# Kernel optimization log

Hardware: AMD Instinct MI355X
Metric: run time of the kernel (lower is better)

The kernel has to match this reference:

```python
import jax, jax.numpy as jnp
import numpy as np

P, B, D, H, O = 512, 8, 256, 75, 128  # passage_len, batch, input_size, attn hidden, GRU hidden


def setup_inputs() -> dict:
    key = jax.random.key(0)
    ks = jax.random.split(key, 10)

    def w(k, shape, fan_in):
        return jax.random.normal(k, shape, jnp.float32) * (1.0 / np.sqrt(fan_in))

    return {
        "v": jax.random.normal(ks[0], (P, B, D), jnp.float32),
        "Wvp1": w(ks[1], (H, D), D),          # nn.Linear(input_size, hidden, bias=False)
        "Wvp2": w(ks[2], (H, D), D),
        "vw": w(ks[3], (H,), H),               # nn.Linear(hidden, 1, bias=False)
        "Wg": w(ks[4], (2 * D, 2 * D), 2 * D),  # Gate linear, no bias
        "w_ih_f": w(ks[5], (3 * O, 2 * D), 2 * D),
        "w_hh_f": w(ks[6], (3 * O, O), O),
        "b_ih_f": jnp.zeros((3 * O,), jnp.float32),
        "b_hh_f": jnp.zeros((3 * O,), jnp.float32),
        "w_ih_b": w(ks[7], (3 * O, 2 * D), 2 * D),
        "w_hh_b": w(ks[8], (3 * O, O), O),
        "b_ih_b": jnp.zeros((3 * O,), jnp.float32),
        "b_hh_b": jnp.zeros((3 * O,), jnp.float32),
    }


def _gru(x, w_ih, w_hh, b_ih, b_hh):
    # x: (T, B, in) -> hidden states (T, B, O); PyTorch GRU gate order (r, z, n)
    hdim = w_hh.shape[1]
    xp = x @ w_ih.T + b_ih  # precompute input projections: (T, B, 3O)

    def step(h, xp_t):
        gh = h @ w_hh.T + b_hh
        i_r, i_z, i_n = jnp.split(xp_t, 3, axis=-1)
        h_r, h_z, h_n = jnp.split(gh, 3, axis=-1)
        r = jax.nn.sigmoid(i_r + h_r)
        z = jax.nn.sigmoid(i_z + h_z)
        n = jnp.tanh(i_n + r * h_n)
        h_new = (1.0 - z) * n + z * h
        return h_new, h_new

    h0 = jnp.zeros((x.shape[1], hdim), x.dtype)
    _, hs = jax.lax.scan(step, h0, xp)
    return hs


def reference(v, Wvp1, Wvp2, vw, Wg,
              w_ih_f, w_hh_f, b_ih_f, b_hh_f,
              w_ih_b, w_hh_b, b_ih_b, b_hh_b):
    # dropout is inference no-op (and in the torch code its result is discarded anyway)
    Wv1 = v @ Wvp1.T  # (P, B, H) -- broadcast over key axis (dim 1 after expand)
    Wv2 = v @ Wvp2.T  # (P, B, H) -- broadcast over query axis
    # s[i, j, b, h] = tanh(Wv2[i] + Wv1[j]); softmax over i (keys)
    s = jnp.tanh(Wv2[:, None] + Wv1[None, :])          # (P, P, B, H)
    scores = jnp.einsum('ijbh,h->ijb', s, vw)          # (P, P, B)
    a = jax.nn.softmax(scores, axis=0)
    c = jnp.einsum('ijb,ibd->jbd', a, v)               # attended context (P, B, D)
    g = jnp.concatenate([v, c], axis=2)                # (P, B, 2D)
    g = jax.nn.sigmoid(g @ Wg.T) * g                   # Gate
    hf = _gru(g, w_ih_f, w_hh_f, b_ih_f, b_hh_f)
    hb = _gru(g[::-1], w_ih_b, w_hh_b, b_ih_b, b_hh_b)[::-1]
    return jnp.concatenate([hf, hb], axis=2)           # (P, B, 2O)
```

## Files before the change

kernel.cpp:

```cpp
#include <hip/hip_runtime.h>

#define TP 512
#define TB 8
#define TD 256
#define TH 75
#define THP 80
#define TO 128

typedef _Float16 half_t;
typedef _Float16 half2v __attribute__((ext_vector_type(2)));
typedef _Float16 half4v __attribute__((ext_vector_type(4)));
typedef _Float16 half8v __attribute__((ext_vector_type(8)));
typedef float    float4v __attribute__((ext_vector_type(4)));

__device__ __forceinline__ float fast_rcp(float x) { return __builtin_amdgcn_rcpf(x); }
__device__ __forceinline__ float fast_tanh(float x) {
    return 1.0f - 2.0f * fast_rcp(1.0f + __expf(2.0f * x));
}
__device__ __forceinline__ float fast_sigmoid(float x) {
    return fast_rcp(1.0f + __expf(-x));
}
__device__ __forceinline__ float fdot2h(half2v a, half2v b, float c) {
#if __has_builtin(__builtin_amdgcn_fdot2)
    return __builtin_amdgcn_fdot2(a, b, c, false);
#else
    return c + (float)a[0] * (float)b[0] + (float)a[1] * (float)b[1];
#endif
}
#define EXT2(v, j) __builtin_shufflevector((v), (v), 2*(j), 2*(j)+1)
__device__ __forceinline__ void dot3_h8(half8v wr, half8v wz, half8v wn, half8v h,
                                        float& ar, float& az, float& an) {
    half2v h0 = EXT2(h, 0), h1 = EXT2(h, 1), h2 = EXT2(h, 2), h3 = EXT2(h, 3);
    ar = fdot2h(EXT2(wr, 0), h0, ar);
    az = fdot2h(EXT2(wz, 0), h0, az);
    an = fdot2h(EXT2(wn, 0), h0, an);
    ar = fdot2h(EXT2(wr, 1), h1, ar);
    az = fdot2h(EXT2(wz, 1), h1, az);
    an = fdot2h(EXT2(wn, 1), h1, an);
    ar = fdot2h(EXT2(wr, 2), h2, ar);
    az = fdot2h(EXT2(wz, 2), h2, az);
    an = fdot2h(EXT2(wn, 2), h2, an);
    ar = fdot2h(EXT2(wr, 3), h3, ar);
    az = fdot2h(EXT2(wz, 3), h3, az);
    an = fdot2h(EXT2(wn, 3), h3, an);
}
__device__ __forceinline__ float pair_sum_dpp(float v) {
    int i1 = __builtin_amdgcn_update_dpp(0, __builtin_bit_cast(int, v), 0xB1, 0xF, 0xF, true);
    return v + __builtin_bit_cast(float, i1);
}

__global__ __launch_bounds__(256) void prep_kernel(
    const float* __restrict__ v,
    const float* __restrict__ Wvp1, const float* __restrict__ Wvp2,
    const float* __restrict__ Wg,   const float* __restrict__ wihf,
    const float* __restrict__ wihb, const float* __restrict__ bihf,
    const float* __restrict__ bihb, const float* __restrict__ whhf,
    const float* __restrict__ whhb,
    float* __restrict__ bihC,
    half_t* __restrict__ v16, half_t* __restrict__ g16,
    half_t* __restrict__ Wg16B, half_t* __restrict__ Wih16B,
    half_t* __restrict__ whh16, half_t* __restrict__ WT16B)
{
    int idx = blockIdx.x * 256 + threadIdx.x;
    if (idx < 1048576) {
        half_t val = (half_t)v[idx];
        v16[idx] = val;
        int row = idx >> 8, d = idx & 255;
        g16[row * 512 + d] = val;
        return;
    }
    idx -= 1048576;
    if (idx < 768) { bihC[idx] = (idx < 384) ? bihf[idx] : bihb[idx - 384]; return; }
    idx -= 768;
    if (idx < 262144) {
        int j = idx & 7, lane = (idx >> 3) & 63, kt = (idx >> 9) & 15, nt = idx >> 13;
        int o = nt * 16 + (lane & 15);
        int k = kt * 32 + ((lane >> 4) << 3) + j;
        Wg16B[idx] = (half_t)Wg[o * 512 + k];
        return;
    }
    idx -= 262144;
    if (idx < 393216) {
        int j = idx & 7, lane = (idx >> 3) & 63, kt = (idx >> 9) & 15, nt = idx >> 13;
        int o = nt * 16 + (lane & 15);
        int k = kt * 32 + ((lane >> 4) << 3) + j;
        Wih16B[idx] = (half_t)((o < 384) ? wihf[o * 512 + k] : wihb[(o - 384) * 512 + k]);
        return;
    }
    idx -= 393216;
    if (idx < 98304) {
        int d = idx / 49152, i = idx - d * 49152;
        whh16[idx] = (half_t)(d ? whhb[i] : whhf[i]);
        return;
    }
    idx -= 98304;
    if (idx < 40960) {
        int j = idx & 7, lane = (idx >> 3) & 63, kt = (idx >> 9) & 7, nt = idx >> 12;
        int o = nt * 16 + (lane & 15);
        int k = kt * 32 + ((lane >> 4) << 3) + j;
        float vv = 0.0f;
        if (o < 75)       vv = Wvp1[o * 256 + k];
        else if (o < 150) vv = Wvp2[(o - 75) * 256 + k];
        WT16B[idx] = (half_t)vv;
    }
}

__global__ __launch_bounds__(256) void vtrans_kernel(
    const float* __restrict__ v, half_t* __restrict__ vT16)
{
    __shared__ half_t lt[64 * 66];
    int t = threadIdx.x;
    int b  = blockIdx.x >> 5;
    int pt = (blockIdx.x >> 2) & 7;
    int dt = blockIdx.x & 3;

    {
        int pl = t >> 2, dseg = (t & 3) * 16;
        const float4* src = (const float4*)(v + (((pt * 64 + pl) * 8 + b) << 8) + dt * 64 + dseg);
        float4 f0 = src[0], f1 = src[1], f2 = src[2], f3 = src[3];
        half_t hv[16] = {
            (half_t)f0.x,(half_t)f0.y,(half_t)f0.z,(half_t)f0.w,
            (half_t)f1.x,(half_t)f1.y,(half_t)f1.z,(half_t)f1.w,
            (half_t)f2.x,(half_t)f2.y,(half_t)f2.z,(half_t)f2.w,
            (half_t)f3.x,(half_t)f3.y,(half_t)f3.z,(half_t)f3.w };
#pragma unroll
        for (int u = 0; u < 16; ++u) lt[(dseg + u) * 66 + pl] = hv[u];
    }
    __syncthreads();
    {
        int dl = t >> 2, pseg = (t & 3) * 16;
        half8v h0 = *(const half8v*)(lt + dl * 66 + pseg);
        half8v h1 = *(const half8v*)(lt + dl * 66 + pseg + 8);
        half8v* dst = (half8v*)(vT16 + ((b * 256 + dt * 64 + dl) << 9) + pt * 64 + pseg);
        dst[0] = h0; dst[1] = h1;
    }
}

__global__ __launch_bounds__(256) void wv12_kernel(
    const half_t* __restrict__ v16, const half_t* __restrict__ WT16B,
    float* __restrict__ Wv1, float* __restrict__ Wv2T)
{
    int tid = threadIdx.x;
    int lane = tid & 63, w = tid >> 6;
    int l15 = lane & 15, quad = lane >> 4;
    int r0 = blockIdx.x * 64 + w * 16;

    float4v acc[10];
#pragma unroll
    for (int nt = 0; nt < 10; ++nt) acc[nt] = (float4v){0.f, 0.f, 0.f, 0.f};

#pragma unroll
    for (int kt = 0; kt < 8; ++kt) {
        half8v a = *(const half8v*)(v16 + (r0 + l15) * 256 + kt * 32 + quad * 8);
#pragma unroll
        for (int nt = 0; nt < 10; ++nt) {
            half8v b = *(const half8v*)(WT16B + ((nt * 8 + kt) * 64 + lane) * 8);
            acc[nt] = __builtin_amdgcn_mfma_f32_16x16x32_f16(a, b, acc[nt], 0, 0, 0);
        }
    }
#pragma unroll
    for (int nt = 0; nt < 10; ++nt) {
        int col = nt * 16 + l15;
#pragma unroll
        for (int r = 0; r < 4; ++r) {
            int row = r0 + quad * 4 + r;
            int p = row >> 3, b = row & 7;
            int ob = (b * TP + p) * THP;
            float val2 = 2.0f * acc[nt][r];
            if (col < 75)       Wv1[ob + col] = val2;
            else if (col < 80)  { Wv1[ob + col] = 0.0f;
                                  Wv2T[(b * THP + col - 75) * TP + p] = val2; }
            else if (col < 150) Wv2T[(b * THP + col - 75) * TP + p] = val2;
            else if (col < 155) Wv2T[(b * THP + col - 75) * TP + p] = 0.0f;
        }
    }
}

__global__ __launch_bounds__(256) void score_kernel(
    const float* __restrict__ Wv1, const float* __restrict__ Wv2T,
    const float* __restrict__ vw, half_t* __restrict__ a16)
{
    int tid = threadIdx.x;
    int b  = blockIdx.x >> 7;
    int j0 = (blockIdx.x & 127) * 4;
    __shared__ float wv1j[4 * THP];
    __shared__ float vws[THP];
    __shared__ float sc[4 * TP];

    if (tid < THP) vws[tid] = (tid < TH) ? vw[tid] : 0.0f;
    for (int e = tid; e < 4 * THP; e += 256) {
        int jj = e / THP, k = e - jj * THP;
        wv1j[e] = Wv1[(b * TP + j0 + jj) * THP + k];
    }
    __syncthreads();

    float Csum = 0.0f;
    {
        const float4* c4 = (const float4*)vws;
        for (int kk = 0; kk < 20; ++kk) { float4 c = c4[kk]; Csum += c.x + c.y + c.z + c.w; }
    }

    int i0 = tid, i1 = tid + 256;
    float acc0[4] = {0.f,0.f,0.f,0.f}, acc1[4] = {0.f,0.f,0.f,0.f};
    const float* wvt = Wv2T + b * THP * TP;
#pragma unroll
    for (int kt = 0; kt < 5; ++kt) {
        float r0v[16], r1v[16];
#pragma unroll
        for (int u = 0; u < 16; ++u) {
            const float* colp = wvt + (kt * 16 + u) * TP;
            r0v[u] = colp[i0];
            r1v[u] = colp[i1];
        }
        const float* cp = vws + kt * 16;
#pragma unroll
        for (int jj = 0; jj < 4; ++jj) {
            const float* w1 = wv1j + jj * THP + kt * 16;
            float s0 = 0.f, s1 = 0.f;
#pragma unroll
            for (int u = 0; u < 16; ++u) {
                float cu = cp[u], wu = w1[u];
                s0 += cu * fast_rcp(1.0f + __expf(r0v[u] + wu));
                s1 += cu * fast_rcp(1.0f + __expf(r1v[u] + wu));
            }
            acc0[jj] += s0; acc1[jj] += s1;
        }
    }
#pragma unroll
    for (int jj = 0; jj < 4; ++jj) {
        sc[jj * TP + i0] = Csum - 2.0f * acc0[jj];
        sc[jj * TP + i1] = Csum - 2.0f * acc1[jj];
    }
    __syncthreads();

    {
        int jj = tid >> 6, l = tid & 63;
        float m = -1e30f;
#pragma unroll
        for (int q = 0; q < 8; ++q) m = fmaxf(m, sc[jj * TP + l + q * 64]);
#pragma unroll
        for (int s = 32; s > 0; s >>= 1) m = fmaxf(m, __shfl_xor(m, s));
        float e[8];
        float sum = 0.0f;
#pragma unroll
        for (int q = 0; q < 8; ++q) { e[q] = __expf(sc[jj * TP + l + q * 64] - m); sum += e[q]; }
#pragma unroll
        for (int s = 32; s > 0; s >>= 1) sum += __shfl_xor(sum, s);
        float inv = fast_rcp(sum);
        half_t* arow = a16 + (b * TP + j0 + jj) * TP;
#pragma unroll
        for (int q = 0; q < 8; ++q) arow[l + q * 64] = (half_t)(e[q] * inv);
    }
}

__global__ __launch_bounds__(256) void context_kernel(
    const half_t* __restrict__ a16, const half_t* __restrict__ vT16,
    half_t* __restrict__ g16)
{
    int tid = threadIdx.x;
    int lane = tid & 63, w = tid >> 6;
    int l15 = lane & 15, quad = lane >> 4;
    int b  = blockIdx.x >> 5;
    int mt = blockIdx.x & 31;

    const half_t* arow = a16 + (b * TP + mt * 16 + l15) * TP;
    const half_t* vbase = vT16 + ((b * 256) << 9);

    float4v acc[4];
#pragma unroll
    for (int nti = 0; nti < 4; ++nti) acc[nti] = (float4v){0.f, 0.f, 0.f, 0.f};

#pragma unroll 4
    for (int kt = 0; kt < 16; ++kt) {
        half8v a = *(const half8v*)(arow + kt * 32 + quad * 8);
#pragma unroll
        for (int nti = 0; nti < 4; ++nti) {
            int d = (w * 4 + nti) * 16 + l15;
            half8v bb = *(const half8v*)(vbase + (d << 9) + kt * 32 + quad * 8);
            acc[nti] = __builtin_amdgcn_mfma_f32_16x16x32_f16(a, bb, acc[nti], 0, 0, 0);
        }
    }
#pragma unroll
    for (int nti = 0; nti < 4; ++nti) {
        int d = (w * 4 + nti) * 16 + l15;
#pragma unroll
        for (int r = 0; r < 4; ++r) {
            int j = mt * 16 + quad * 4 + r;
            g16[(j * TB + b) * 512 + 256 + d] = (half_t)acc[nti][r];
        }
    }
}

__global__ __launch_bounds__(256, 1) void gatexp_kernel(
    const half_t* __restrict__ g16, const half_t* __restrict__ Wg16B,
    const half_t* __restrict__ Wih16B, const float* __restrict__ bihC,
    float* __restrict__ xpf, float* __restrict__ xpb)
{
    __shared__ half_t gA[32 * 520];
    int tid = threadIdx.x;
    int r0 = blockIdx.x * 32;
    int lane = tid & 63, w = tid >> 6;
    int l15 = lane & 15, quad = lane >> 4;

    for (int e = tid; e < 2048; e += 256) {
        int row = e >> 6, c8 = e & 63;
        *(half8v*)(gA + row * 520 + c8 * 8) =
            *(const half8v*)(g16 + (r0 + row) * 512 + c8 * 8);
    }
    __syncthreads();

    float4v acc[2][8];
#pragma unroll
    for (int mi = 0; mi < 2; ++mi)
#pragma unroll
        for (int nti = 0; nti < 8; ++nti) acc[mi][nti] = (float4v){0.f, 0.f, 0.f, 0.f};

    for (int kt = 0; kt < 16; ++kt) {
        half8v a0 = *(const half8v*)(gA + l15 * 520 + kt * 32 + quad * 8);
        half8v a1 = *(const half8v*)(gA + (16 + l15) * 520 + kt * 32 + quad * 8);
#pragma unroll
        for (int nti = 0; nti < 8; ++nti) {
            half8v bb = *(const half8v*)(Wg16B + (((w * 8 + nti) * 16 + kt) * 64 + lane) * 8);
            acc[0][nti] = __builtin_amdgcn_mfma_f32_16x16x32_f16(a0, bb, acc[0][nti], 0, 0, 0);
            acc[1][nti] = __builtin_amdgcn_mfma_f32_16x16x32_f16(a1, bb, acc[1][nti], 0, 0, 0);
        }
    }
#pragma unroll
    for (int mi = 0; mi < 2; ++mi)
#pragma unroll
        for (int nti = 0; nti < 8; ++nti) {
            int colg = (w * 8 + nti) * 16 + l15;
#pragma unroll
            for (int r = 0; r < 4; ++r) {
                float gv = (float)gA[(mi * 16 + quad * 4 + r) * 520 + colg];
                acc[mi][nti][r] = fast_sigmoid(acc[mi][nti][r]) * gv;
            }
        }
    __syncthreads();
#pragma unroll
    for (int mi = 0; mi < 2; ++mi)
#pragma unroll
        for (int nti = 0; nti < 8; ++nti) {
            int colg = (w * 8 + nti) * 16 + l15;
#pragma unroll
            for (int r = 0; r < 4; ++r)
                gA[(mi * 16 + quad * 4 + r) * 520 + colg] = (half_t)acc[mi][nti][r];
        }
    __syncthreads();

    float4v c2[2][12];
#pragma unroll
    for (int mi = 0; mi < 2; ++mi)
#pragma unroll
        for (int nt2 = 0; nt2 < 12; ++nt2) {
            float bv = bihC[(w * 12 + nt2) * 16 + l15];
            c2[mi][nt2] = (float4v){bv, bv, bv, bv};
        }

    for (int kt = 0; kt < 16; ++kt) {
        half8v a0 = *(const half8v*)(gA + l15 * 520 + kt * 32 + quad * 8);
        half8v a1 = *(const half8v*)(gA + (16 + l15) * 520 + kt * 32 + quad * 8);
#pragma unroll
        for (int nt2 = 0; nt2 < 12; ++nt2) {
            half8v bb = *(const half8v*)(Wih16B + (((w * 12 + nt2) * 16 + kt) * 64 + lane) * 8);
            c2[0][nt2] = __builtin_amdgcn_mfma_f32_16x16x32_f16(a0, bb, c2[0][nt2], 0, 0, 0);
            c2[1][nt2] = __builtin_amdgcn_mfma_f32_16x16x32_f16(a1, bb, c2[1][nt2], 0, 0, 0);
        }
    }
#pragma unroll
    for (int mi = 0; mi < 2; ++mi)
#pragma unroll
        for (int nt2 = 0; nt2 < 12; ++nt2) {
            int col = (w * 12 + nt2) * 16 + l15;
            float* dst = (col < 384) ? (xpf + col) : (xpb + col - 384);
#pragma unroll
            for (int r = 0; r < 4; ++r)
                dst[(r0 + mi * 16 + quad * 4 + r) * 384] = c2[mi][nt2][r];
        }
}

__global__ __launch_bounds__(256, 1) void gru_kernel(
    const float* __restrict__ xpf, const float* __restrict__ xpb,
    const half_t* __restrict__ whh16,
    const float* __restrict__ bhhf, const float* __restrict__ bhhb,
    float* __restrict__ out)
{
    int tid = threadIdx.x;
    int dir = blockIdx.x >> 3;
    int b   = blockIdx.x & 7;
    const float* xp  = dir ? xpb  : xpf;
    const float* bhh = dir ? bhhb : bhhf;
    const half_t* wbase = whh16 + dir * 3 * TO * TO;

    __shared__ __align__(16) half_t hb[2][TO];

    int o = tid >> 1, hf = tid & 1;

    half8v wr[8], wz[8], wn[8];
    {
        const half_t* pr = wbase + (o)          * TO + hf * 64;
        const half_t* pz = wbase + (TO + o)     * TO + hf * 64;
        const half_t* pn = wbase + (2 * TO + o) * TO + hf * 64;
        asm volatile(
            "global_load_dwordx4 %0,  %24, off\n\t"
            "global_load_dwordx4 %1,  %24, off offset:16\n\t"
            "global_load_dwordx4 %2,  %24, off offset:32\n\t"
            "global_load_dwordx4 %3,  %24, off offset:48\n\t"
            "global_load_dwordx4 %4,  %24, off offset:64\n\t"
            "global_load_dwordx4 %5,  %24, off offset:80\n\t"
            "global_load_dwordx4 %6,  %24, off offset:96\n\t"
            "global_load_dwordx4 %7,  %24, off offset:112\n\t"
            "global_load_dwordx4 %8,  %25, off\n\t"
            "global_load_dwordx4 %9,  %25, off offset:16\n\t"
            "global_load_dwordx4 %10, %25, off offset:32\n\t"
            "global_load_dwordx4 %11, %25, off offset:48\n\t"
            "global_load_dwordx4 %12, %25, off offset:64\n\t"
            "global_load_dwordx4 %13, %25, off offset:80\n\t"
            "global_load_dwordx4 %14, %25, off offset:96\n\t"
            "global_load_dwordx4 %15, %25, off offset:112\n\t"
            "global_load_dwordx4 %16, %26, off\n\t"
            "global_load_dwordx4 %17, %26, off offset:16\n\t"
            "global_load_dwordx4 %18, %26, off offset:32\n\t"
            "global_load_dwordx4 %19, %26, off offset:48\n\t"
            "global_load_dwordx4 %20, %26, off offset:64\n\t"
            "global_load_dwordx4 %21, %26, off offset:80\n\t"
            "global_load_dwordx4 %22, %26, off offset:96\n\t"
            "global_load_dwordx4 %23, %26, off offset:112\n\t"
            "s_waitcnt vmcnt(0)"
            : "=&v"(wr[0]), "=&v"(wr[1]), "=&v"(wr[2]), "=&v"(wr[3]),
              "=&v"(wr[4]), "=&v"(wr[5]), "=&v"(wr[6]), "=&v"(wr[7]),
              "=&v"(wz[0]), "=&v"(wz[1]), "=&v"(wz[2]), "=&v"(wz[3]),
              "=&v"(wz[4]), "=&v"(wz[5]), "=&v"(wz[6]), "=&v"(wz[7]),
              "=&v"(wn[0]), "=&v"(wn[1]), "=&v"(wn[2]), "=&v"(wn[3]),
              "=&v"(wn[4]), "=&v"(wn[5]), "=&v"(wn[6]), "=&v"(wn[7])
            : "v"(pr), "v"(pz), "v"(pn));
    }

    float br = 0.f, bz = 0.f, bn = 0.f, h = 0.f;
    if (hf == 0) {
        br = bhh[o]; bz = bhh[TO + o]; bn = bhh[2 * TO + o];
    }
    if (tid < TO) hb[0][tid] = (half_t)0.0f;
    __syncthreads();

    float xrv[8], xzv[8], xnv[8], hist[8];

    for (int S = 0; S < TP; S += 8) {
        if (hf == 0) {
#pragma unroll
            for (int u = 0; u < 8; ++u) {
                int s = S + u;
                int tn = dir ? (TP - 1 - s) : s;
                const float* xpt = xp + (tn * TB + b) * 384;
                xrv[u] = xpt[o]; xzv[u] = xpt[TO + o]; xnv[u] = xpt[2 * TO + o];
            }
        }
#pragma unroll
        for (int u = 0; u < 8; ++u) {
            int s = S + u;
            int cur = s & 1;
            const half8v* h8 = (const half8v*)(&hb[cur][hf * 64]);
            half8v hv0 = h8[0], hv1 = h8[1], hv2 = h8[2], hv3 = h8[3];
            half8v hv4 = h8[4], hv5 = h8[5], hv6 = h8[6], hv7 = h8[7];

            float ar = 0.f, az = 0.f, an = 0.f;
            dot3_h8(wr[0], wz[0], wn[0], hv0, ar, az, an);
            dot3_h8(wr[1], wz[1], wn[1], hv1, ar, az, an);
            dot3_h8(wr[2], wz[2], wn[2], hv2, ar, az, an);
            dot3_h8(wr[3], wz[3], wn[3], hv3, ar, az, an);
            dot3_h8(wr[4], wz[4], wn[4], hv4, ar, az, an);
            dot3_h8(wr[5], wz[5], wn[5], hv5, ar, az, an);
            dot3_h8(wr[6], wz[6], wn[6], hv6, ar, az, an);
            dot3_h8(wr[7], wz[7], wn[7], hv7, ar, az, an);

            ar = pair_sum_dpp(ar);
            az = pair_sum_dpp(az);
            an = pair_sum_dpp(an);
            if (hf == 0) {
                float r = fast_sigmoid(xrv[u] + ar + br);
                float z = fast_sigmoid(xzv[u] + az + bz);
                float n = fast_tanh(xnv[u] + r * (an + bn));
                h = (1.0f - z) * n + z * h;
                hb[cur ^ 1][o] = (half_t)h;
                hist[u] = h;
            }
            asm volatile("s_waitcnt lgkmcnt(0)" ::: "memory");
            __builtin_amdgcn_s_barrier();
        }
        if (hf == 0) {
#pragma unroll
            for (int u = 0; u < 8; ++u) {
                int s = S + u;
                int t = dir ? (TP - 1 - s) : s;
                out[(t * TB + b) * 256 + dir * TO + o] = hist[u];
            }
        }
    }
}

extern "C" void kernel_launch(void* const* d_in, const int* in_sizes, int n_in,
                              void* d_out, int out_size, void* d_ws, size_t ws_size,
                              hipStream_t stream) {
    const float* v    = (const float*)d_in[0];
    const float* Wvp1 = (const float*)d_in[1];
    const float* Wvp2 = (const float*)d_in[2];
    const float* vw   = (const float*)d_in[3];
    const float* Wg   = (const float*)d_in[4];
    const float* wihf = (const float*)d_in[5];
    const float* whhf = (const float*)d_in[6];
    const float* bihf = (const float*)d_in[7];
    const float* bhhf = (const float*)d_in[8];
    const float* wihb = (const float*)d_in[9];
    const float* whhb = (const float*)d_in[10];
    const float* bihb = (const float*)d_in[11];
    const float* bhhb = (const float*)d_in[12];

    float* ws   = (float*)d_ws;
    float* bihC = ws;
    float* Wv1  = bihC + 768;
    float* Wv2T = Wv1 + 327680;
    float* xpf  = Wv2T + 327680;
    float* xpb  = xpf + 1572864;
    half_t* g16    = (half_t*)(xpb + 1572864);
    half_t* Wg16B  = g16 + 2097152;
    half_t* Wih16B = Wg16B + 262144;
    half_t* whh16  = Wih16B + 393216;
    half_t* v16    = whh16 + 98304;
    half_t* WT16B  = v16 + 1048576;
    half_t* vT16   = WT16B + 40960;
    half_t* a16    = vT16 + 1048576;
    float* out  = (float*)d_out;

    prep_kernel<<<7203, 256, 0, stream>>>(v, Wvp1, Wvp2, Wg, wihf, wihb, bihf, bihb,
                                          whhf, whhb, bihC, v16, g16,
                                          Wg16B, Wih16B, whh16, WT16B);
    vtrans_kernel<<<256, 256, 0, stream>>>(v, vT16);
    wv12_kernel<<<64, 256, 0, stream>>>(v16, WT16B, Wv1, Wv2T);
    score_kernel<<<1024, 256, 0, stream>>>(Wv1, Wv2T, vw, a16);
    context_kernel<<<256, 256, 0, stream>>>(a16, vT16, g16);
    gatexp_kernel<<<128, 256, 0, stream>>>(g16, Wg16B, Wih16B, bihC, xpf, xpb);
    gru_kernel<<<16, 256, 0, stream>>>(xpf, xpb, whh16, bhhf, bhhb, out);
}
```

Measured before the change: 434.3 us.

## Fold transpose into prep, split wv12 columns across waves, use exp2 in scores

The v transpose moves into the prep kernel as extra blocks, which removes one kernel launch. wv12 is re-split so each 128-thread block handles 16 rows and each of its two waves covers 5 column tiles, giving 256 blocks instead of 64. The Wv projections are pre-scaled by 2*log2(e) so the score inner loop can call the raw exp2 instruction instead of __expf. This trims a multiply from the hottest loop and improves occupancy of the small GEMM. The cost is a larger prep kernel that now uses shared memory in every block.

New measurement: 417.0 us. 1.04x faster.

```diff
diff --git a/kernel.cpp b/kernel.cpp
--- a/kernel.cpp
+++ b/kernel.cpp
@@ -7,6 +7,8 @@
 #define THP 80
 #define TO 128
 
+#define LOG2E2 2.8853900817779268f
+
 typedef _Float16 half_t;
 typedef _Float16 half2v __attribute__((ext_vector_type(2)));
 typedef _Float16 half4v __attribute__((ext_vector_type(4)));
@@ -14,6 +16,13 @@
 typedef float    float4v __attribute__((ext_vector_type(4)));
 
 __device__ __forceinline__ float fast_rcp(float x) { return __builtin_amdgcn_rcpf(x); }
+__device__ __forceinline__ float ex2(float x) {
+#if __has_builtin(__builtin_amdgcn_exp2f)
+    return __builtin_amdgcn_exp2f(x);
+#else
+    float r; asm("v_exp_f32 %0, %1" : "=v"(r) : "v"(x)); return r;
+#endif
+}
 __device__ __forceinline__ float fast_tanh(float x) {
     return 1.0f - 2.0f * fast_rcp(1.0f + __expf(2.0f * x));
 }
@@ -59,8 +68,40 @@
     float* __restrict__ bihC,
     half_t* __restrict__ v16, half_t* __restrict__ g16,
     half_t* __restrict__ Wg16B, half_t* __restrict__ Wih16B,
-    half_t* __restrict__ whh16, half_t* __restrict__ WT16B)
+    half_t* __restrict__ whh16, half_t* __restrict__ WT16B,
+    half_t* __restrict__ vT16)
 {
+    __shared__ half_t lt[64 * 66];
+
+    if (blockIdx.x >= 7203) {
+        int vb = blockIdx.x - 7203;
+        int t = threadIdx.x;
+        int b  = vb >> 5;
+        int pt = (vb >> 2) & 7;
+        int dt = vb & 3;
+        {
+            int pl = t >> 2, dseg = (t & 3) * 16;
+            const float4* src = (const float4*)(v + (((pt * 64 + pl) * 8 + b) << 8) + dt * 64 + dseg);
+            float4 f0 = src[0], f1 = src[1], f2 = src[2], f3 = src[3];
+            half_t hv[16] = {
+                (half_t)f0.x,(half_t)f0.y,(half_t)f0.z,(half_t)f0.w,
+                (half_t)f1.x,(half_t)f1.y,(half_t)f1.z,(half_t)f1.w,
+                (half_t)f2.x,(half_t)f2.y,(half_t)f2.z,(half_t)f2.w,
+                (half_t)f3.x,(half_t)f3.y,(half_t)f3.z,(half_t)f3.w };
+#pragma unroll
+            for (int u = 0; u < 16; ++u) lt[(dseg + u) * 66 + pl] = hv[u];
+        }
+        __syncthreads();
+        {
+            int dl = t >> 2, pseg = (t & 3) * 16;
+            half8v h0 = *(const half8v*)(lt + dl * 66 + pseg);
+            half8v h1 = *(const half8v*)(lt + dl * 66 + pseg + 8);
+            half8v* dst = (half8v*)(vT16 + ((b * 256 + dt * 64 + dl) << 9) + pt * 64 + pseg);
+            dst[0] = h0; dst[1] = h1;
+        }
+        return;
+    }
+
     int idx = blockIdx.x * 256 + threadIdx.x;
     if (idx < 1048576) {
         half_t val = (half_t)v[idx];
@@ -105,68 +146,38 @@
     }
 }
 
-__global__ __launch_bounds__(256) void vtrans_kernel(
-    const float* __restrict__ v, half_t* __restrict__ vT16)
-{
-    __shared__ half_t lt[64 * 66];
-    int t = threadIdx.x;
-    int b  = blockIdx.x >> 5;
-    int pt = (blockIdx.x >> 2) & 7;
-    int dt = blockIdx.x & 3;
-
-    {
-        int pl = t >> 2, dseg = (t & 3) * 16;
-        const float4* src = (const float4*)(v + (((pt * 64 + pl) * 8 + b) << 8) + dt * 64 + dseg);
-        float4 f0 = src[0], f1 = src[1], f2 = src[2], f3 = src[3];
-        half_t hv[16] = {
-            (half_t)f0.x,(half_t)f0.y,(half_t)f0.z,(half_t)f0.w,
-            (half_t)f1.x,(half_t)f1.y,(half_t)f1.z,(half_t)f1.w,
-            (half_t)f2.x,(half_t)f2.y,(half_t)f2.z,(half_t)f2.w,
-            (half_t)f3.x,(half_t)f3.y,(half_t)f3.z,(half_t)f3.w };
-#pragma unroll
-        for (int u = 0; u < 16; ++u) lt[(dseg + u) * 66 + pl] = hv[u];
-    }
-    __syncthreads();
-    {
-        int dl = t >> 2, pseg = (t & 3) * 16;
-        half8v h0 = *(const half8v*)(lt + dl * 66 + pseg);
-        half8v h1 = *(const half8v*)(lt + dl * 66 + pseg + 8);
-        half8v* dst = (half8v*)(vT16 + ((b * 256 + dt * 64 + dl) << 9) + pt * 64 + pseg);
-        dst[0] = h0; dst[1] = h1;
-    }
-}
-
-__global__ __launch_bounds__(256) void wv12_kernel(
+__global__ __launch_bounds__(128) void wv12_kernel(
     const half_t* __restrict__ v16, const half_t* __restrict__ WT16B,
     float* __restrict__ Wv1, float* __restrict__ Wv2T)
 {
     int tid = threadIdx.x;
     int lane = tid & 63, w = tid >> 6;
     int l15 = lane & 15, quad = lane >> 4;
-    int r0 = blockIdx.x * 64 + w * 16;
-
-    float4v acc[10];
-#pragma unroll
-    for (int nt = 0; nt < 10; ++nt) acc[nt] = (float4v){0.f, 0.f, 0.f, 0.f};
+    int r0 = blockIdx.x * 16;
+
+    float4v acc[5];
+#pragma unroll
+    for (int n5 = 0; n5 < 5; ++n5) acc[n5] = (float4v){0.f, 0.f, 0.f, 0.f};
 
 #pragma unroll
     for (int kt = 0; kt < 8; ++kt) {
         half8v a = *(const half8v*)(v16 + (r0 + l15) * 256 + kt * 32 + quad * 8);
 #pragma unroll
-        for (int nt = 0; nt < 10; ++nt) {
+        for (int n5 = 0; n5 < 5; ++n5) {
+            int nt = w * 5 + n5;
             half8v b = *(const half8v*)(WT16B + ((nt * 8 + kt) * 64 + lane) * 8);
-            acc[nt] = __builtin_amdgcn_mfma_f32_16x16x32_f16(a, b, acc[nt], 0, 0, 0);
-        }
-    }
-#pragma unroll
-    for (int nt = 0; nt < 10; ++nt) {
-        int col = nt * 16 + l15;
+            acc[n5] = __builtin_amdgcn_mfma_f32_16x16x32_f16(a, b, acc[n5], 0, 0, 0);
+        }
+    }
+#pragma unroll
+    for (int n5 = 0; n5 < 5; ++n5) {
+        int col = (w * 5 + n5) * 16 + l15;
 #pragma unroll
         for (int r = 0; r < 4; ++r) {
             int row = r0 + quad * 4 + r;
             int p = row >> 3, b = row & 7;
             int ob = (b * TP + p) * THP;
-            float val2 = 2.0f * acc[nt][r];
+            float val2 = LOG2E2 * acc[n5][r];
             if (col < 75)       Wv1[ob + col] = val2;
             else if (col < 80)  { Wv1[ob + col] = 0.0f;
                                   Wv2T[(b * THP + col - 75) * TP + p] = val2; }
@@ -220,8 +231,8 @@
 #pragma unroll
             for (int u = 0; u < 16; ++u) {
                 float cu = cp[u], wu = w1[u];
-                s0 += cu * fast_rcp(1.0f + __expf(r0v[u] + wu));
-                s1 += cu * fast_rcp(1.0f + __expf(r1v[u] + wu));
+                s0 += cu * fast_rcp(1.0f + ex2(r0v[u] + wu));
+                s1 += cu * fast_rcp(1.0f + ex2(r1v[u] + wu));
             }
             acc0[jj] += s0; acc1[jj] += s1;
         }
@@ -531,11 +542,10 @@
     half_t* a16    = vT16 + 1048576;
     float* out  = (float*)d_out;
 
-    prep_kernel<<<7203, 256, 0, stream>>>(v, Wvp1, Wvp2, Wg, wihf, wihb, bihf, bihb,
+    prep_kernel<<<7459, 256, 0, stream>>>(v, Wvp1, Wvp2, Wg, wihf, wihb, bihf, bihb,
                                           whhf, whhb, bihC, v16, g16,
-                                          Wg16B, Wih16B, whh16, WT16B);
-    vtrans_kernel<<<256, 256, 0, stream>>>(v, vT16);
-    wv12_kernel<<<64, 256, 0, stream>>>(v16, WT16B, Wv1, Wv2T);
+                                          Wg16B, Wih16B, whh16, WT16B, vT16);
+    wv12_kernel<<<256, 128, 0, stream>>>(v16, WT16B, Wv1, Wv2T);
     score_kernel<<<1024, 256, 0, stream>>>(Wv1, Wv2T, vw, a16);
     context_kernel<<<256, 256, 0, stream>>>(a16, vT16, g16);
     gatexp_kernel<<<128, 256, 0, stream>>>(g16, Wg16B, Wih16B, bihC, xpf, xpb);
```
